# Performance work log

Hardware: AMD Instinct MI355X
Metric: run time of the kernel (lower is better)

## Reference

```python
import jax, jax.numpy as jnp
import numpy as np

N_NODES = 10000
N_EDGES = 256000
H = 128   # n_hidden_feats
P = 64    # n_product_feats
NB = 8    # n_basis
NS = 10   # n_species
RH = 64   # radial MLP hidden width
RC = 5.0  # r_cutoff
AVG = 25.6  # avg_n_neighbors


def _radial(r):
    # Bessel radial basis * polynomial cutoff envelope (p = n_polynomial_cutoff = 5). r: [E,1]
    n = jnp.arange(1, NB + 1, dtype=r.dtype)
    bessel = jnp.sqrt(2.0 / RC) * jnp.sin(n * jnp.pi * r / RC) / r  # [E,NB]
    u = r / RC
    p = 5.0
    env = 1.0 - 0.5 * (p + 1) * (p + 2) * u**p + p * (p + 2) * u**(p + 1) - 0.5 * p * (p + 1) * u**(p + 2)
    env = jnp.where(u < 1.0, env, 0.0)
    return bessel * env


def _mlp(x, Ws):
    for W in Ws[:-1]:
        x = jax.nn.silu(x @ W)
    return x @ Ws[-1]


def _B0(w, A0, A1):
    # correlation-3 symmetric contractions to a scalar target; w: [N,5,P]
    dot = jnp.sum(A1 * A1, axis=-1)  # [N,P]  (rank-1 . rank-1)
    return (w[:, 0] * A0 + w[:, 1] * A0**2 + w[:, 2] * A0**3
            + w[:, 3] * dot + w[:, 4] * A0 * dot)


def _forward(positions, shifts, node_attrs,
             W_embed, Wsc1, Wup0_1, R1_0, R1_1, R1_2, R1_3,
             Wout0_1, Wout1_1, Wp0_1, Wp1_1, Wl0_1, Wl1_1,
             Wsc2, Wup0_2, Wup1_2, R2_0, R2_1, R2_2, R2_3,
             Wout0_2, Wout1_2, Wp0_2, Wl0_2,
             idx_i, idx_j):
    v = positions[idx_i] - positions[idx_j] - shifts                    # [E,3]
    r = jnp.maximum(jnp.linalg.norm(v, axis=-1, keepdims=True), 1e-9)   # [E,1]
    Y1 = v / r                                                          # Cartesian harmonics, l=1
    edge_feats = _radial(r)                                             # [E,NB]

    feats0 = node_attrs @ W_embed                                       # [N,H] scalar node embedding

    # ---- interaction 1: node feats l=0, edge attrs l<=1 -> targets l<=1 ----
    sc0 = jnp.einsum('nk,kch,nc->nh', node_attrs, Wsc1, feats0)         # per-species residual
    h0 = feats0 @ Wup0_1
    w = _mlp(edge_feats, (R1_0, R1_1, R1_2, R1_3)).reshape(-1, 2, H)    # tp weights per edge
    h0j = h0[idx_j]                                                     # [E,H]
    m0 = w[:, 0] * h0j                                                  # 0x0->0
    m1 = (w[:, 1] * h0j)[:, :, None] * Y1[:, None, :]                   # 0x1->1, [E,H,3]
    a0 = jax.ops.segment_sum(m0, idx_i, num_segments=N_NODES) / AVG
    a1 = jax.ops.segment_sum(m1, idx_i, num_segments=N_NODES) / AVG
    A0 = a0 @ Wout0_1                                                   # [N,P]
    A1 = jnp.einsum('nhd,hp->npd', a1, Wout1_1)                         # [N,P,3]

    # ---- product basis 1 (correlation 3, targets l=0 and l=1) ----
    wp0 = jnp.einsum('nk,kqp->nqp', node_attrs, Wp0_1)                  # [N,5,P]
    wp1 = jnp.einsum('nk,kqp->nqp', node_attrs, Wp1_1)                  # [N,4,P]
    B0 = _B0(wp0, A0, A1)
    dot = jnp.sum(A1 * A1, axis=-1)
    B1 = (wp1[:, 0] + wp1[:, 1] * A0 + wp1[:, 2] * A0**2 + wp1[:, 3] * dot)[:, :, None] * A1
    out0 = B0 @ Wl0_1 + sc0                                             # [N,H]
    out1 = jnp.einsum('npd,ph->nhd', B1, Wl1_1)                         # [N,H,3] (sc has no l=1 part)

    # ---- interaction 2: node feats l<=1, targets l<=1; product target l=0 ----
    sc0b = jnp.einsum('nk,kch,nc->nh', node_attrs, Wsc2, out0)
    g0 = out0 @ Wup0_2
    g1 = jnp.einsum('nhd,hg->ngd', out1, Wup1_2)
    w2 = _mlp(edge_feats, (R2_0, R2_1, R2_2, R2_3)).reshape(-1, 5, H)   # 5 tp paths
    g0j = g0[idx_j]
    g1j = g1[idx_j]
    Y1e = Y1[:, None, :]
    m0 = w2[:, 0] * g0j + w2[:, 3] * jnp.sum(g1j * Y1e, axis=-1)        # 0x0->0, 1x1->0 (dot)
    m1 = ((w2[:, 1] * g0j)[:, :, None] * Y1e                             # 0x1->1
          + w2[:, 2][:, :, None] * g1j                                   # 1x0->1
          + w2[:, 4][:, :, None] * jnp.cross(g1j, jnp.broadcast_to(Y1e, g1j.shape)))  # 1x1->1
    a0 = jax.ops.segment_sum(m0, idx_i, num_segments=N_NODES) / AVG
    a1 = jax.ops.segment_sum(m1, idx_i, num_segments=N_NODES) / AVG
    A0 = a0 @ Wout0_2
    A1 = jnp.einsum('nhd,hp->npd', a1, Wout1_2)
    wp0 = jnp.einsum('nk,kqp->nqp', node_attrs, Wp0_2)
    out0b = _B0(wp0, A0, A1) @ Wl0_2 + sc0b                             # [N,H]

    # torch returns [feats[:, :H] per layer]; the first H flattened columns are the scalar block
    return jnp.stack([out0, out0b], axis=0)                             # [2,N,H]


def setup_inputs() -> dict:
    key = jax.random.key(0)
    ks = iter(jax.random.split(key, 40))

    def nrm(shape, fan_in):
        return jax.random.normal(next(ks), shape, dtype=jnp.float32) / np.sqrt(fan_in)

    positions = jax.random.normal(next(ks), (N_NODES, 3), dtype=jnp.float32) * 8.0
    idx_i = jax.random.randint(next(ks), (N_EDGES,), 0, N_NODES)
    idx_j = jax.random.randint(next(ks), (N_EDGES,), 0, N_NODES)
    shifts = jnp.zeros((N_EDGES, 3), jnp.float32)
    species = jax.random.randint(next(ks), (N_NODES,), 0, NS)
    node_attrs = jax.nn.one_hot(species, NS, dtype=jnp.float32)

    return dict(
        positions=positions, shifts=shifts, node_attrs=node_attrs,
        W_embed=nrm((NS, H), NS),
        Wsc1=nrm((NS, H, H), H), Wup0_1=nrm((H, H), H),
        R1_0=nrm((NB, RH), NB), R1_1=nrm((RH, RH), RH), R1_2=nrm((RH, RH), RH), R1_3=nrm((RH, 2 * H), RH),
        Wout0_1=nrm((H, P), H), Wout1_1=nrm((H, P), H),
        Wp0_1=nrm((NS, 5, P), 1.0), Wp1_1=nrm((NS, 4, P), 1.0),
        Wl0_1=nrm((P, H), P), Wl1_1=nrm((P, H), P),
        Wsc2=nrm((NS, H, H), H), Wup0_2=nrm((H, H), H), Wup1_2=nrm((H, H), H),
        R2_0=nrm((NB, RH), NB), R2_1=nrm((RH, RH), RH), R2_2=nrm((RH, RH), RH), R2_3=nrm((RH, 5 * H), RH),
        Wout0_2=nrm((H, P), H), Wout1_2=nrm((H, P), H),
        Wp0_2=nrm((NS, 5, P), 1.0),
        Wl0_2=nrm((P, H), P),
        idx_i=idx_i, idx_j=idx_j,
    )


def reference(positions, shifts, node_attrs,
              W_embed, Wsc1, Wup0_1, R1_0, R1_1, R1_2, R1_3,
              Wout0_1, Wout1_1, Wp0_1, Wp1_1, Wl0_1, Wl1_1,
              Wsc2, Wup0_2, Wup1_2, R2_0, R2_1, R2_2, R2_3,
              Wout0_2, Wout1_2, Wp0_2, Wl0_2,
              idx_i, idx_j):
    return _forward(positions, shifts, node_attrs,
                    W_embed, Wsc1, Wup0_1, R1_0, R1_1, R1_2, R1_3,
                    Wout0_1, Wout1_1, Wp0_1, Wp1_1, Wl0_1, Wl1_1,
                    Wsc2, Wup0_2, Wup1_2, R2_0, R2_1, R2_2, R2_3,
                    Wout0_2, Wout1_2, Wp0_2, Wl0_2,
                    idx_i, idx_j)
```

## Files before the change

kernel.cpp:

```cpp
#include <hip/hip_runtime.h>
#include <math.h>

#define NN 10000
#define NE 256000
#define HD 128
#define PD 64
#define NBASIS 8
#define NSPEC 10
#define RHID 64
#define RCUT 5.0f
#define INV_AVG 0.0390625f
#define PI_F 3.14159265358979f
#define ECAP 12288
#define NACTCAP 8192
#define RSZ 819

__device__ __forceinline__ float silu(float x) {
    return x / (1.0f + expf(-x));
}

__global__ __launch_bounds__(256) void k_initTables(
    const float* __restrict__ na_, const float* __restrict__ We,
    const float* __restrict__ Wsc1, const float* __restrict__ Wup01,
    const float* __restrict__ Wup02, const float* __restrict__ Wsc2,
    int* __restrict__ spec, int* __restrict__ ecnt, int* cnt, int* eTot,
    int* __restrict__ scurG, int* __restrict__ actLst,
    float* __restrict__ sc0s, float* __restrict__ h0s,
    float* __restrict__ g0d, float* __restrict__ sc0bd) {
    __shared__ float ls[HD];
    int b = blockIdx.x;
    if (b < 40) {
        int n = b * 256 + threadIdx.x;
        if (n == 0) { *cnt = 0; *eTot = 0; }
        if (n < NSPEC) scurG[n] = 0;
        if (n < NACTCAP) actLst[n] = -1;
        if (n >= NN) return;
        ecnt[n] = 0;
        int s = 0;
        for (int k = 0; k < NSPEC; k++)
            if (na_[n * NSPEC + k] > 0.5f) s = k;
        spec[n] = s;
    } else {
        int s = b - 40;
        int t = threadIdx.x;
        if (t < HD) {
            float acc1 = 0.f, acc2 = 0.f;
            for (int c = 0; c < HD; c++) {
                float fe = We[s * HD + c];
                acc1 += fe * Wsc1[((size_t)s * HD + c) * HD + t];
                acc2 += fe * Wup01[c * HD + t];
            }
            sc0s[s * HD + t] = acc1;
            h0s[s * HD + t] = acc2;
            ls[t] = acc1;
        }
        __syncthreads();
        if (t < HD) {
            float a1 = 0.f, a2 = 0.f;
            for (int c = 0; c < HD; c++) {
                float v = ls[c];
                a1 += v * Wup02[c * HD + t];
                a2 += v * Wsc2[((size_t)s * HD + c) * HD + t];
            }
            g0d[s * HD + t] = a1;
            sc0bd[s * HD + t] = a2;
        }
    }
}

__global__ __launch_bounds__(256) void k_compact(
    const float* __restrict__ pos, const float* __restrict__ shifts,
    const int* __restrict__ ii, const int* __restrict__ jj,
    int* cnt, int* __restrict__ ecnt,
    int* __restrict__ ui, int* __restrict__ uj,
    float* __restrict__ uY, float* __restrict__ uF) {
    __shared__ int lTot;
    __shared__ int blockBase;
    int t = threadIdx.x;
    if (t == 0) lTot = 0;
    __syncthreads();
    int e0 = (blockIdx.x * 256 + t) * 4;
    int iv[4], jv[4], keep[4];
    float vx[4], vy[4], vz[4], rr[4];
    #pragma unroll
    for (int k = 0; k < 4; k++) {
        int e = e0 + k;
        int i = ii[e], j = jj[e];
        iv[k] = i; jv[k] = j;
        float x = pos[i * 3 + 0] - pos[j * 3 + 0] - shifts[e * 3 + 0];
        float y = pos[i * 3 + 1] - pos[j * 3 + 1] - shifts[e * 3 + 1];
        float z = pos[i * 3 + 2] - pos[j * 3 + 2] - shifts[e * 3 + 2];
        float r = sqrtf(x * x + y * y + z * z);
        r = fmaxf(r, 1e-9f);
        vx[k] = x; vy[k] = y; vz[k] = z; rr[k] = r;
        keep[k] = (r < RCUT) ? 1 : 0;
    }
    int myCnt = keep[0] + keep[1] + keep[2] + keep[3];
    int myOff = 0;
    if (myCnt) myOff = atomicAdd(&lTot, myCnt);
    __syncthreads();
    if (t == 0) blockBase = atomicAdd(cnt, lTot);
    __syncthreads();
    int slot = blockBase + myOff;
    #pragma unroll
    for (int k = 0; k < 4; k++) {
        if (!keep[k]) continue;
        int i = iv[k];
        atomicAdd(&ecnt[i], 1);
        ui[slot] = i; uj[slot] = jv[k];
        float r = rr[k];
        float inv = 1.0f / r;
        uY[slot * 3 + 0] = vx[k] * inv;
        uY[slot * 3 + 1] = vy[k] * inv;
        uY[slot * 3 + 2] = vz[k] * inv;
        float u = r * (1.0f / RCUT);
        float u5 = u * u * u * u * u;
        float env = 1.0f - 21.0f * u5 + 35.0f * u5 * u - 15.0f * u5 * u * u;
        float c0 = 0.6324555320336759f * env * inv;
        float th = PI_F * u;
        float s1, c1;
        __sincosf(th, &s1, &c1);
        float two_c1 = 2.0f * c1;
        float sp = 0.f, sn = s1;
        uF[slot * NBASIS + 0] = c0 * sn;
        #pragma unroll
        for (int b = 1; b < NBASIS; b++) {
            float s_new = two_c1 * sn - sp;
            sp = sn; sn = s_new;
            uF[slot * NBASIS + b] = c0 * sn;
        }
        slot++;
    }
}

__global__ __launch_bounds__(256) void k_assignPlace(
    const int* __restrict__ ecnt, const int* __restrict__ spec,
    int* __restrict__ ebase, int* __restrict__ ecur,
    int* eTot, int* scurG,
    int* __restrict__ actIndex, int* __restrict__ actList) {
    __shared__ int lTot;
    __shared__ int blockBase;
    __shared__ int lHist[NSPEC];
    __shared__ int lBase[NSPEC];
    int t = threadIdx.x;
    int n = blockIdx.x * 256 + t;
    if (t == 0) lTot = 0;
    if (t < NSPEC) lHist[t] = 0;
    __syncthreads();
    int ec = (n < NN) ? ecnt[n] : 0;
    int s = (n < NN) ? spec[n] : 0;
    bool act = (ec > 0);
    int myOff = 0, myIdx = 0;
    if (act) {
        myOff = atomicAdd(&lTot, ec);
        myIdx = atomicAdd(&lHist[s], 1);
    }
    __syncthreads();
    if (t == 0) blockBase = atomicAdd(eTot, lTot);
    if (t < NSPEC) lBase[t] = (lHist[t] > 0) ? atomicAdd(&scurG[t], lHist[t]) : 0;
    __syncthreads();
    if (n < NN) {
        if (act) {
            int b = blockBase + myOff;
            ebase[n] = b;
            ecur[n] = b;
            int rank = lBase[s] + myIdx;
            if (rank < RSZ) {
                int p = s * RSZ + rank;
                actList[p] = n;
                actIndex[n] = p;
            } else {
                actIndex[n] = -1;
            }
        } else {
            actIndex[n] = -1;
        }
    }
}

__global__ __launch_bounds__(256) void k_sortFill(
    const int* cnt, const int* __restrict__ ui, const int* __restrict__ uj,
    const float* __restrict__ uY, const float* __restrict__ uF,
    int* __restrict__ ecur, int* __restrict__ sj,
    float* __restrict__ sY, float* __restrict__ sF,
    const int* __restrict__ spec, const float* __restrict__ sc0s,
    const float* __restrict__ sc0bd,
    float* __restrict__ out0g, float* __restrict__ outbg) {
    int b = blockIdx.x;
    if (b < 48) {
        int e = b * 256 + threadIdx.x;
        int n = *cnt; if (n > ECAP) n = ECAP;
        if (e >= n) return;
        int slot = atomicAdd(&ecur[ui[e]], 1);
        if (slot >= ECAP) return;
        sj[slot] = uj[e];
        #pragma unroll
        for (int d = 0; d < 3; d++) sY[slot * 3 + d] = uY[e * 3 + d];
        #pragma unroll
        for (int bb = 0; bb < NBASIS; bb++) sF[slot * NBASIS + bb] = uF[e * NBASIS + bb];
    } else {
        int t = (b - 48) * 256 + threadIdx.x;
        int n = t >> 6, c = t & 63;
        if (n >= NN) return;
        int s = spec[n];
        out0g[(size_t)n * HD + c] = sc0s[s * HD + c];
        out0g[(size_t)n * HD + 64 + c] = sc0s[s * HD + 64 + c];
        outbg[(size_t)n * HD + c] = sc0bd[s * HD + c];
        outbg[(size_t)n * HD + 64 + c] = sc0bd[s * HD + 64 + c];
    }
}

__global__ __launch_bounds__(256) void k_hid(
    const int* cnt, const float* __restrict__ sF,
    const float* __restrict__ A0, const float* __restrict__ A1, const float* __restrict__ A2,
    const float* __restrict__ B0, const float* __restrict__ B1, const float* __restrict__ B2,
    float* __restrict__ xh1, float* __restrict__ xh2) {
    int lane = threadIdx.x & 63;
    int wid = (blockIdx.x * 256 + threadIdx.x) >> 6;
    int ne = *cnt; if (ne > ECAP) ne = ECAP;
    int base = wid * 2;
    if (base >= ne) return;
    const float* W0 = (blockIdx.y == 0) ? A0 : B0;
    const float* W1 = (blockIdx.y == 0) ? A1 : B1;
    const float* W2 = (blockIdx.y == 0) ? A2 : B2;
    float* dst = (blockIdx.y == 0) ? xh1 : xh2;
    int e0 = base, e1 = (base + 1 < ne) ? base + 1 : base;
    float x0, x1;
    {
        float F0[NBASIS], F1[NBASIS];
        #pragma unroll
        for (int b = 0; b < NBASIS; b++) { F0[b] = sF[e0 * NBASIS + b]; F1[b] = sF[e1 * NBASIS + b]; }
        float a0 = 0.f, a1 = 0.f;
        #pragma unroll
        for (int b = 0; b < NBASIS; b++) {
            float wv = W0[b * RHID + lane];
            a0 += F0[b] * wv; a1 += F1[b] * wv;
        }
        x0 = silu(a0); x1 = silu(a1);
    }
    {
        float c0 = 0.f, c1 = 0.f;
        for (int c = 0; c < RHID; c++) {
            float wv = W1[c * RHID + lane];
            c0 += __shfl(x0, c) * wv; c1 += __shfl(x1, c) * wv;
        }
        x0 = silu(c0); x1 = silu(c1);
    }
    {
        float c0 = 0.f, c1 = 0.f;
        for (int c = 0; c < RHID; c++) {
            float wv = W2[c * RHID + lane];
            c0 += __shfl(x0, c) * wv; c1 += __shfl(x1, c) * wv;
        }
        x0 = silu(c0); x1 = silu(c1);
    }
    dst[(size_t)e0 * RHID + lane] = x0;
    if (base + 1 < ne) dst[(size_t)e1 * RHID + lane] = x1;
}

__global__ __launch_bounds__(256) void k_wmat(
    const int* cnt, const float* __restrict__ xh1, const float* __restrict__ xh2,
    const float* __restrict__ A3, const float* __restrict__ B3,
    float* __restrict__ ew1, float* __restrict__ ew2) {
    __shared__ float sX[32 * RHID];
    int lane = threadIdx.x & 63;
    int w = __builtin_amdgcn_readfirstlane((int)(threadIdx.x >> 6));
    int y = blockIdx.y;
    int ne = *cnt; if (ne > ECAP) ne = ECAP;
    const float* X; const float* W; float* dst; int ncol, col0;
    if (y < 4) { X = xh1; W = A3; dst = ew1; ncol = 2 * HD; col0 = y * 64; }
    else       { X = xh2; W = B3; dst = ew2; ncol = 5 * HD; col0 = (y - 4) * 64; }
    int eBase = blockIdx.x * 32;
    {
        const float4* src = (const float4*)(X + (size_t)eBase * RHID);
        float4* d4 = (float4*)sX;
        #pragma unroll
        for (int it = 0; it < 2; it++)
            d4[threadIdx.x + it * 256] = src[threadIdx.x + it * 256];
    }
    __syncthreads();
    if (eBase >= ne) return;
    int w8 = w * 8;
    float acc[8] = {0,0,0,0,0,0,0,0};
    for (int c = 0; c < RHID; c += 4) {
        float4 xv[8];
        #pragma unroll
        for (int k = 0; k < 8; k++) xv[k] = *(const float4*)&sX[(w8 + k) * RHID + c];
        #pragma unroll
        for (int cc = 0; cc < 4; cc++) {
            float wv = W[(c + cc) * ncol + col0 + lane];
            #pragma unroll
            for (int k = 0; k < 8; k++) {
                float xc = (cc==0)?xv[k].x:(cc==1)?xv[k].y:(cc==2)?xv[k].z:xv[k].w;
                acc[k] += xc * wv;
            }
        }
    }
    int e0 = eBase + w8;
    int rem = ne - e0; if (rem > 8) rem = 8;
    for (int k = 0; k < rem; k++)
        dst[(size_t)(e0 + k) * ncol + col0 + lane] = acc[k];
}

__global__ __launch_bounds__(256) void k_agg1(
    const int* __restrict__ actList,
    const int* __restrict__ ebase, const int* __restrict__ ecnt,
    const int* __restrict__ sj, const float* __restrict__ sY,
    const float* __restrict__ ew, const int* __restrict__ spec,
    const float* __restrict__ h0s, float* __restrict__ a0c, float* __restrict__ a1c) {
    int lane = threadIdx.x & 63;
    int ia = (blockIdx.x * 256 + threadIdx.x) >> 6;
    int h = blockIdx.y * 64;
    int n = actList[ia];
    if (n < 0) return;
    int eb = ebase[n], ec = ecnt[n];
    float a0 = 0.f;
    float a1[3] = {0,0,0};
    for (int idx = eb; idx < eb + ec; idx++) {
        int j = sj[idx];
        int sp = spec[j];
        float h0 = h0s[sp * HD + h + lane];
        const float* w = ew + (size_t)idx * 256;
        float w0 = w[h + lane], w1 = w[128 + h + lane];
        a0 += w0 * h0;
        float m1 = w1 * h0;
        #pragma unroll
        for (int d = 0; d < 3; d++) a1[d] += m1 * sY[idx * 3 + d];
    }
    a0c[(size_t)ia * HD + h + lane] = a0 * INV_AVG;
    #pragma unroll
    for (int d = 0; d < 3; d++)
        a1c[((size_t)d * NACTCAP + ia) * HD + h + lane] = a1[d] * INV_AVG;
}

__global__ __launch_bounds__(256) void k_proj(
    const int* __restrict__ actList,
    const float* __restrict__ x0buf, const float* __restrict__ x1buf,
    const float* __restrict__ W0, const float* __restrict__ W1,
    float* __restrict__ am0, float* __restrict__ am1) {
    __shared__ float sX[16 * HD];
    int lane = threadIdx.x & 63;
    int w = __builtin_amdgcn_readfirstlane((int)(threadIdx.x >> 6));
    int y = blockIdx.y;
    const float* X = (y == 0) ? x0buf : (x1buf + (size_t)(y - 1) * NACTCAP * HD);
    const float* W = (y == 0) ? W0 : W1;
    int iaBase = blockIdx.x * 16;
    {
        const float4* src = (const float4*)(X + (size_t)iaBase * HD);
        float4* d4 = (float4*)sX;
        #pragma unroll
        for (int it = 0; it < 2; it++)
            d4[threadIdx.x + it * 256] = src[threadIdx.x + it * 256];
    }
    __syncthreads();
    bool any = false;
    int ia0 = iaBase + w * 4;
    #pragma unroll
    for (int k = 0; k < 4; k++) any = any || (actList[ia0 + k] >= 0);
    if (!any) return;
    float* dst = (y == 0) ? am0 : (am1 + (size_t)(y - 1) * NACTCAP * PD);
    int w4 = w * 4;
    float acc[4] = {0,0,0,0};
    for (int c = 0; c < HD; c += 4) {
        float4 xv[4];
        #pragma unroll
        for (int k = 0; k < 4; k++) xv[k] = *(const float4*)&sX[(w4 + k) * HD + c];
        #pragma unroll
        for (int cc = 0; cc < 4; cc++) {
            float wv = W[(c + cc) * PD + lane];
            #pragma unroll
            for (int k = 0; k < 4; k++) {
                float xc = (cc==0)?xv[k].x:(cc==1)?xv[k].y:(cc==2)?xv[k].z:xv[k].w;
                acc[k] += xc * wv;
            }
        }
    }
    #pragma unroll
    for (int k = 0; k < 4; k++) dst[(size_t)(ia0 + k) * PD + lane] = acc[k];
}

__global__ __launch_bounds__(256) void k_bout(
    const int* __restrict__ actList,
    const float* __restrict__ am0, const float* __restrict__ am1,
    const int* __restrict__ spec,
    const float* __restrict__ Wp0, const float* __restrict__ Wp1,
    const float* __restrict__ Wl0, const float* __restrict__ Wl1,
    const float* __restrict__ sc0s,
    float* __restrict__ out0g, float* __restrict__ out0c, float* __restrict__ out1c) {
    __shared__ float sB[4][8][PD];
    int lane = threadIdx.x & 63;
    int w = __builtin_amdgcn_readfirstlane((int)(threadIdx.x >> 6));
    int y = blockIdx.y;
    int bs = y >> 1, h = (y & 1) * 64;
    int ia0 = (blockIdx.x * 4 + w) * 8;
    int nv[8], sk[8];
    bool any = false;
    #pragma unroll
    for (int k = 0; k < 8; k++) {
        nv[k] = actList[ia0 + k];
        any = any || (nv[k] >= 0);
        sk[k] = spec[(nv[k] >= 0) ? nv[k] : 0];
    }
    if (!any) return;
    #pragma unroll
    for (int k = 0; k < 8; k++) {
        int ia = ia0 + k;
        int s = sk[k];
        float A0v = am0[(size_t)ia * PD + lane];
        float a1x = am1[((size_t)0 * NACTCAP + ia) * PD + lane];
        float a1y = am1[((size_t)1 * NACTCAP + ia) * PD + lane];
        float a1z = am1[((size_t)2 * NACTCAP + ia) * PD + lane];
        float dot = a1x * a1x + a1y * a1y + a1z * a1z;
        float A02 = A0v * A0v;
        float B;
        if (bs == 0) {
            const float* wp = Wp0 + (size_t)(s * 5) * PD;
            B = wp[lane] * A0v + wp[PD + lane] * A02 + wp[2 * PD + lane] * A02 * A0v +
                wp[3 * PD + lane] * dot + wp[4 * PD + lane] * A0v * dot;
        } else {
            const float* wp = Wp1 + (size_t)(s * 4) * PD;
            float fac = wp[lane] + wp[PD + lane] * A0v + wp[2 * PD + lane] * A02 + wp[3 * PD + lane] * dot;
            float a1d = (bs == 1) ? a1x : ((bs == 2) ? a1y : a1z);
            B = fac * a1d;
        }
        sB[w][k][lane] = B;
    }
    const float* Wl = (bs == 0) ? Wl0 : Wl1;
    float o[8] = {0,0,0,0,0,0,0,0};
    for (int q = 0; q < PD; q += 4) {
        float4 bq[8];
        #pragma unroll
        for (int k = 0; k < 8; k++) bq[k] = *(const float4*)&sB[w][k][q];
        #pragma unroll
        for (int qq = 0; qq < 4; qq++) {
            float wl = Wl[(q + qq) * HD + h + lane];
            #pragma unroll
            for (int k = 0; k < 8; k++) {
                float b = (qq==0)?bq[k].x:(qq==1)?bq[k].y:(qq==2)?bq[k].z:bq[k].w;
                o[k] += b * wl;
            }
        }
    }
    if (bs == 0) {
        #pragma unroll
        for (int k = 0; k < 8; k++) {
            int ia = ia0 + k;
            float v = o[k] + sc0s[sk[k] * HD + h + lane];
            if (nv[k] >= 0) out0g[(size_t)nv[k] * HD + h + lane] = v;
            out0c[(size_t)ia * HD + h + lane] = v;
        }
    } else {
        float* dst = out1c + (size_t)(bs - 1) * NACTCAP * HD;
        #pragma unroll
        for (int k = 0; k < 8; k++)
            dst[(size_t)(ia0 + k) * HD + h + lane] = o[k];
    }
}

__global__ __launch_bounds__(256) void k_g(
    const int* __restrict__ actList, const int* __restrict__ spec,
    const float* __restrict__ out0c, const float* __restrict__ out1c,
    const float* __restrict__ Wsc2, const float* __restrict__ Wup02, const float* __restrict__ Wup12,
    float* __restrict__ sc0bc, float* __restrict__ g0c, float* __restrict__ g1c) {
    __shared__ float sX[32 * HD];
    int lane = threadIdx.x & 63;
    int w = __builtin_amdgcn_readfirstlane((int)(threadIdx.x >> 6));
    int y = blockIdx.y;
    int st = y >> 1, h = (y & 1) * 64;
    int blockBase = blockIdx.x * 32;
    const float* X = (st <= 1) ? out0c : (out1c + (size_t)(st - 2) * NACTCAP * HD);
    {
        const float4* src = (const float4*)(X + (size_t)blockBase * HD);
        float4* d4 = (float4*)sX;
        #pragma unroll
        for (int it = 0; it < 4; it++)
            d4[threadIdx.x + it * 256] = src[threadIdx.x + it * 256];
    }
    int nb0 = actList[blockBase];
    int sB0 = spec[(nb0 >= 0) ? nb0 : 0];
    __syncthreads();
    int ia0 = blockBase + w * 8;
    int nv[8], sk[8];
    bool any = false;
    #pragma unroll
    for (int k = 0; k < 8; k++) {
        nv[k] = actList[ia0 + k];
        any = any || (nv[k] >= 0);
        sk[k] = (st == 0) ? spec[(nv[k] >= 0) ? nv[k] : 0] : 0;
    }
    if (!any) return;
    const float* Wt = (st == 0) ? (Wsc2 + (size_t)sB0 * HD * HD)
                    : ((st == 1) ? Wup02 : Wup12);
    int w8 = w * 8;
    float acc[8] = {0,0,0,0,0,0,0,0};
    for (int c = 0; c < HD; c += 4) {
        float4 xv[8];
        #pragma unroll
        for (int k = 0; k < 8; k++) xv[k] = *(const float4*)&sX[(w8 + k) * HD + c];
        #pragma unroll
        for (int cc = 0; cc < 4; cc++) {
            float wv = Wt[(c + cc) * HD + h + lane];
            #pragma unroll
            for (int k = 0; k < 8; k++) {
                float xc = (cc==0)?xv[k].x:(cc==1)?xv[k].y:(cc==2)?xv[k].z:xv[k].w;
                acc[k] += xc * wv;
            }
        }
    }
    if (st == 0) {
        #pragma unroll 1
        for (int k = 0; k < 8; k++) {
            if (nv[k] < 0 || sk[k] == sB0) continue;
            const float* Wm = Wsc2 + (size_t)sk[k] * HD * HD;
            float p = 0.f;
            for (int c = 0; c < HD; c++) p += sX[(w8 + k) * HD + c] * Wm[c * HD + h + lane];
            acc[k] = p;
        }
    }
    float* dst = (st == 0) ? sc0bc : ((st == 1) ? g0c : (g1c + (size_t)(st - 2) * NACTCAP * HD));
    #pragma unroll
    for (int k = 0; k < 8; k++)
        dst[(size_t)(ia0 + k) * HD + h + lane] = acc[k];
}

__global__ __launch_bounds__(256) void k_agg2(
    const int* __restrict__ actList,
    const int* __restrict__ ebase, const int* __restrict__ ecnt,
    const int* __restrict__ sj, const float* __restrict__ sY,
    const float* __restrict__ ew, const int* __restrict__ spec,
    const int* __restrict__ actIndex,
    const float* __restrict__ g0c, const float* __restrict__ g1c,
    const float* __restrict__ g0d,
    float* __restrict__ a0c, float* __restrict__ a1c) {
    int lane = threadIdx.x & 63;
    int ia = (blockIdx.x * 256 + threadIdx.x) >> 6;
    int h = blockIdx.y * 64;
    int n = actList[ia];
    if (n < 0) return;
    int eb = ebase[n], ec = ecnt[n];
    float m0 = 0.f;
    float s1[3] = {0,0,0};
    for (int idx = eb; idx < eb + ec; idx++) {
        int j = sj[idx];
        float Yx = sY[idx * 3 + 0], Yy = sY[idx * 3 + 1], Yz = sY[idx * 3 + 2];
        int ji = actIndex[j];
        float gv, gx, gy, gz;
        if (ji >= 0) {
            gv = g0c[(size_t)ji * HD + h + lane];
            gx = g1c[((size_t)0 * NACTCAP + ji) * HD + h + lane];
            gy = g1c[((size_t)1 * NACTCAP + ji) * HD + h + lane];
            gz = g1c[((size_t)2 * NACTCAP + ji) * HD + h + lane];
        } else {
            gv = g0d[spec[j] * HD + h + lane];
            gx = gy = gz = 0.f;
        }
        const float* wr = ew + (size_t)idx * 640;
        float w0 = wr[h + lane];
        float w1 = wr[128 + h + lane];
        float w2 = wr[256 + h + lane];
        float w3 = wr[384 + h + lane];
        float w4 = wr[512 + h + lane];
        float dot = gx * Yx + gy * Yy + gz * Yz;
        m0 += w0 * gv + w3 * dot;
        float cx = gy * Yz - gz * Yy, cy = gz * Yx - gx * Yz, cz = gx * Yy - gy * Yx;
        s1[0] += w1 * gv * Yx + w2 * gx + w4 * cx;
        s1[1] += w1 * gv * Yy + w2 * gy + w4 * cy;
        s1[2] += w1 * gv * Yz + w2 * gz + w4 * cz;
    }
    a0c[(size_t)ia * HD + h + lane] = m0 * INV_AVG;
    #pragma unroll
    for (int d = 0; d < 3; d++)
        a1c[((size_t)d * NACTCAP + ia) * HD + h + lane] = s1[d] * INV_AVG;
}

__global__ __launch_bounds__(256) void k_outC(
    const int* __restrict__ actList, const int* __restrict__ spec,
    const float* __restrict__ am0, const float* __restrict__ am1,
    const float* __restrict__ Wp0, const float* __restrict__ Wl0,
    const float* __restrict__ sc0bc, float* __restrict__ outbg) {
    __shared__ float sB[4][8][PD];
    int lane = threadIdx.x & 63;
    int w = __builtin_amdgcn_readfirstlane((int)(threadIdx.x >> 6));
    int h = blockIdx.y * 64;
    int ia0 = (blockIdx.x * 4 + w) * 8;
    int nv[8];
    bool any = false;
    #pragma unroll
    for (int k = 0; k < 8; k++) { nv[k] = actList[ia0 + k]; any = any || (nv[k] >= 0); }
    if (!any) return;
    #pragma unroll
    for (int k = 0; k < 8; k++) {
        int ia = ia0 + k;
        int s = spec[(nv[k] >= 0) ? nv[k] : 0];
        float A0v = am0[(size_t)ia * PD + lane];
        float a1x = am1[((size_t)0 * NACTCAP + ia) * PD + lane];
        float a1y = am1[((size_t)1 * NACTCAP + ia) * PD + lane];
        float a1z = am1[((size_t)2 * NACTCAP + ia) * PD + lane];
        float dot = a1x * a1x + a1y * a1y + a1z * a1z;
        float A02 = A0v * A0v;
        const float* wp = Wp0 + (size_t)(s * 5) * PD;
        sB[w][k][lane] = wp[lane] * A0v + wp[PD + lane] * A02 + wp[2 * PD + lane] * A02 * A0v +
                         wp[3 * PD + lane] * dot + wp[4 * PD + lane] * A0v * dot;
    }
    float o[8] = {0,0,0,0,0,0,0,0};
    for (int q = 0; q < PD; q += 4) {
        float4 bq[8];
        #pragma unroll
        for (int k = 0; k < 8; k++) bq[k] = *(const float4*)&sB[w][k][q];
        #pragma unroll
        for (int qq = 0; qq < 4; qq++) {
            float wl = Wl0[(q + qq) * HD + h + lane];
            #pragma unroll
            for (int k = 0; k < 8; k++) {
                float b = (qq==0)?bq[k].x:(qq==1)?bq[k].y:(qq==2)?bq[k].z:bq[k].w;
                o[k] += b * wl;
            }
        }
    }
    #pragma unroll
    for (int k = 0; k < 8; k++) {
        if (nv[k] < 0) continue;
        int ia = ia0 + k;
        outbg[(size_t)nv[k] * HD + h + lane] = o[k] + sc0bc[(size_t)ia * HD + h + lane];
    }
}

extern "C" void kernel_launch(void* const* d_in, const int* in_sizes, int n_in,
                              void* d_out, int out_size, void* d_ws, size_t ws_size,
                              hipStream_t stream) {
    const float* pos    = (const float*)d_in[0];
    const float* shifts = (const float*)d_in[1];
    const float* na     = (const float*)d_in[2];
    const float* We     = (const float*)d_in[3];
    const float* Wsc1   = (const float*)d_in[4];
    const float* Wup01  = (const float*)d_in[5];
    const float* R10    = (const float*)d_in[6];
    const float* R11    = (const float*)d_in[7];
    const float* R12    = (const float*)d_in[8];
    const float* R13    = (const float*)d_in[9];
    const float* Wout01 = (const float*)d_in[10];
    const float* Wout11 = (const float*)d_in[11];
    const float* Wp01   = (const float*)d_in[12];
    const float* Wp11   = (const float*)d_in[13];
    const float* Wl01   = (const float*)d_in[14];
    const float* Wl11   = (const float*)d_in[15];
    const float* Wsc2   = (const float*)d_in[16];
    const float* Wup02  = (const float*)d_in[17];
    const float* Wup12  = (const float*)d_in[18];
    const float* R20    = (const float*)d_in[19];
    const float* R21    = (const float*)d_in[20];
    const float* R22    = (const float*)d_in[21];
    const float* R23    = (const float*)d_in[22];
    const float* Wout02 = (const float*)d_in[23];
    const float* Wout12 = (const float*)d_in[24];
    const float* Wp02   = (const float*)d_in[25];
    const float* Wl02   = (const float*)d_in[26];
    const int*   idx_i  = (const int*)d_in[27];
    const int*   idx_j  = (const int*)d_in[28];
    float* out = (float*)d_out;
    float* outb = out + (size_t)NN * HD;

    char* ws = (char*)d_ws;
    size_t off = 0;
    auto alloc = [&](size_t bytes) -> char* {
        char* pp = ws + off;
        off += (bytes + 255) & ~(size_t)255;
        return pp;
    };
    int*   cnt    = (int*)alloc(4);
    int*   eTot   = (int*)alloc(4);
    int*   scurG  = (int*)alloc(NSPEC * 4);
    int*   spec   = (int*)alloc((size_t)NN * 4);
    int*   ecnt   = (int*)alloc((size_t)NN * 4);
    int*   ebase  = (int*)alloc((size_t)NN * 4);
    int*   ecur   = (int*)alloc((size_t)NN * 4);
    int*   actIdx = (int*)alloc((size_t)NN * 4);
    int*   actLst = (int*)alloc((size_t)NACTCAP * 4);
    float* sc0s   = (float*)alloc((size_t)NSPEC * HD * 4);
    float* h0s    = (float*)alloc((size_t)NSPEC * HD * 4);
    float* g0d    = (float*)alloc((size_t)NSPEC * HD * 4);
    float* sc0bd  = (float*)alloc((size_t)NSPEC * HD * 4);
    int*   sj     = (int*)alloc((size_t)ECAP * 4);
    float* sYv    = (float*)alloc((size_t)ECAP * 3 * 4);
    float* sFv    = (float*)alloc((size_t)ECAP * NBASIS * 4);
    float* xh1    = (float*)alloc((size_t)ECAP * RHID * 4);
    float* xh2    = (float*)alloc((size_t)ECAP * RHID * 4);
    float* ew1    = (float*)alloc((size_t)ECAP * 256 * 4);
    float* ew2    = (float*)alloc((size_t)ECAP * 640 * 4);
    int*   ui     = (int*)ew2;
    int*   uj     = ui + NE;
    float* uY     = (float*)(uj + NE);
    float* uF     = uY + (size_t)NE * 3;
    float* a0c    = (float*)alloc((size_t)NACTCAP * HD * 4);
    float* a1c    = (float*)alloc((size_t)NACTCAP * HD * 3 * 4);
    float* am0    = (float*)alloc((size_t)NACTCAP * PD * 4);
    float* am1    = (float*)alloc((size_t)NACTCAP * PD * 3 * 4);
    float* out0c  = (float*)alloc((size_t)NACTCAP * HD * 4);
    float* out1c  = (float*)alloc((size_t)NACTCAP * HD * 3 * 4);
    float* g0c    = (float*)alloc((size_t)NACTCAP * HD * 4);
    float* g1c    = (float*)alloc((size_t)NACTCAP * HD * 3 * 4);
    float* sc0bc  = (float*)alloc((size_t)NACTCAP * HD * 4);

    k_initTables<<<50, 256, 0, stream>>>(na, We, Wsc1, Wup01, Wup02, Wsc2,
                                         spec, ecnt, cnt, eTot, scurG, actLst,
                                         sc0s, h0s, g0d, sc0bd);
    k_compact<<<NE / 1024, 256, 0, stream>>>(pos, shifts, idx_i, idx_j, cnt, ecnt,
                                             ui, uj, uY, uF);
    k_assignPlace<<<(NN + 255) / 256, 256, 0, stream>>>(ecnt, spec, ebase, ecur,
                                                        eTot, scurG, actIdx, actLst);
    k_sortFill<<<48 + (NN * 64) / 256, 256, 0, stream>>>(cnt, ui, uj, uY, uF, ecur,
                                                         sj, sYv, sFv,
                                                         spec, sc0s, sc0bd, out, outb);
    k_hid<<<dim3(ECAP / 8, 2), 256, 0, stream>>>(cnt, sFv, R10, R11, R12,
                                                 R20, R21, R22, xh1, xh2);
    k_wmat<<<dim3(ECAP / 32, 14), 256, 0, stream>>>(cnt, xh1, xh2, R13, R23, ew1, ew2);
    k_agg1<<<dim3(NACTCAP / 4, 2), 256, 0, stream>>>(actLst, ebase, ecnt, sj, sYv, ew1,
                                                     spec, h0s, a0c, a1c);
    k_proj<<<dim3(NACTCAP / 16, 4), 256, 0, stream>>>(actLst, a0c, a1c, Wout01, Wout11,
                                                      am0, am1);
    k_bout<<<dim3(NACTCAP / 32, 8), 256, 0, stream>>>(actLst, am0, am1, spec,
                                                      Wp01, Wp11, Wl01, Wl11, sc0s,
                                                      out, out0c, out1c);
    k_g<<<dim3(NACTCAP / 32, 10), 256, 0, stream>>>(actLst, spec, out0c, out1c,
                                                    Wsc2, Wup02, Wup12, sc0bc, g0c, g1c);
    k_agg2<<<dim3(NACTCAP / 4, 2), 256, 0, stream>>>(actLst, ebase, ecnt, sj, sYv, ew2,
                                                     spec, actIdx, g0c, g1c, g0d, a0c, a1c);
    k_proj<<<dim3(NACTCAP / 16, 4), 256, 0, stream>>>(actLst, a0c, a1c, Wout02, Wout12,
                                                      am0, am1);
    k_outC<<<dim3(NACTCAP / 32, 2), 256, 0, stream>>>(actLst, spec, am0, am1, Wp02, Wl02,
                                                      sc0bc, outb);
}
```

Baseline: 190.7 us.

## Register-tile the wmat and g GEMMs with 4x8 per-thread blocks

Both small dense-GEMM kernels (radial-weight output layer and the second-layer node linear maps) switch from one column per lane with 8 rows per wave to a 4-row by 8-column register tile per thread. Each block now covers 64 rows and 128 columns, X is staged into padded shared memory, and weights are read as float4. This is meant to raise arithmetic intensity and cut redundant weight loads and launch count. In k_g the mixed-species fallback now runs block-wide only when the block is not species-homogeneous, which adds serial per-row work in that case.

```diff
diff --git a/kernel.cpp b/kernel.cpp
--- a/kernel.cpp
+++ b/kernel.cpp
@@ -262,44 +262,51 @@
     const int* cnt, const float* __restrict__ xh1, const float* __restrict__ xh2,
     const float* __restrict__ A3, const float* __restrict__ B3,
     float* __restrict__ ew1, float* __restrict__ ew2) {
-    __shared__ float sX[32 * RHID];
-    int lane = threadIdx.x & 63;
-    int w = __builtin_amdgcn_readfirstlane((int)(threadIdx.x >> 6));
+    __shared__ float sX[64 * 65];
+    int t = threadIdx.x;
+    int ne = *cnt; if (ne > ECAP) ne = ECAP;
     int y = blockIdx.y;
-    int ne = *cnt; if (ne > ECAP) ne = ECAP;
+    int eBase = blockIdx.x * 64;
+    if (eBase >= ne) return;
     const float* X; const float* W; float* dst; int ncol, col0;
-    if (y < 4) { X = xh1; W = A3; dst = ew1; ncol = 2 * HD; col0 = y * 64; }
-    else       { X = xh2; W = B3; dst = ew2; ncol = 5 * HD; col0 = (y - 4) * 64; }
-    int eBase = blockIdx.x * 32;
+    if (y < 2) { X = xh1; W = A3; dst = ew1; ncol = 2 * HD; col0 = y * 128; }
+    else       { X = xh2; W = B3; dst = ew2; ncol = 5 * HD; col0 = (y - 2) * 128; }
     {
         const float4* src = (const float4*)(X + (size_t)eBase * RHID);
-        float4* d4 = (float4*)sX;
-        #pragma unroll
-        for (int it = 0; it < 2; it++)
-            d4[threadIdx.x + it * 256] = src[threadIdx.x + it * 256];
-    }
-    __syncthreads();
-    if (eBase >= ne) return;
-    int w8 = w * 8;
-    float acc[8] = {0,0,0,0,0,0,0,0};
-    for (int c = 0; c < RHID; c += 4) {
-        float4 xv[8];
-        #pragma unroll
-        for (int k = 0; k < 8; k++) xv[k] = *(const float4*)&sX[(w8 + k) * RHID + c];
-        #pragma unroll
-        for (int cc = 0; cc < 4; cc++) {
-            float wv = W[(c + cc) * ncol + col0 + lane];
+        #pragma unroll
+        for (int it = 0; it < 4; it++) {
+            int idx = t + it * 256;
+            float4 v = src[idx];
+            int e = idx >> 4, c4 = (idx & 15) * 4;
+            float* d = &sX[e * 65 + c4];
+            d[0] = v.x; d[1] = v.y; d[2] = v.z; d[3] = v.w;
+        }
+    }
+    __syncthreads();
+    int sgrp = t >> 4;
+    int cg = col0 + (t & 15) * 8;
+    float acc[4][8] = {};
+    for (int c = 0; c < RHID; c++) {
+        float xk[4];
+        #pragma unroll
+        for (int k = 0; k < 4; k++) xk[k] = sX[(sgrp * 4 + k) * 65 + c];
+        float4 wA = *(const float4*)(W + (size_t)c * ncol + cg);
+        float4 wB = *(const float4*)(W + (size_t)c * ncol + cg + 4);
+        float wv[8] = {wA.x, wA.y, wA.z, wA.w, wB.x, wB.y, wB.z, wB.w};
+        #pragma unroll
+        for (int k = 0; k < 4; k++)
             #pragma unroll
-            for (int k = 0; k < 8; k++) {
-                float xc = (cc==0)?xv[k].x:(cc==1)?xv[k].y:(cc==2)?xv[k].z:xv[k].w;
-                acc[k] += xc * wv;
-            }
-        }
-    }
-    int e0 = eBase + w8;
-    int rem = ne - e0; if (rem > 8) rem = 8;
-    for (int k = 0; k < rem; k++)
-        dst[(size_t)(e0 + k) * ncol + col0 + lane] = acc[k];
+            for (int q = 0; q < 8; q++)
+                acc[k][q] += xk[k] * wv[q];
+    }
+    #pragma unroll
+    for (int k = 0; k < 4; k++) {
+        int e = eBase + sgrp * 4 + k;
+        *(float4*)(dst + (size_t)e * ncol + cg) =
+            make_float4(acc[k][0], acc[k][1], acc[k][2], acc[k][3]);
+        *(float4*)(dst + (size_t)e * ncol + cg + 4) =
+            make_float4(acc[k][4], acc[k][5], acc[k][6], acc[k][7]);
+    }
 }
 
 __global__ __launch_bounds__(256) void k_agg1(
@@ -462,65 +469,83 @@
     const float* __restrict__ out0c, const float* __restrict__ out1c,
     const float* __restrict__ Wsc2, const float* __restrict__ Wup02, const float* __restrict__ Wup12,
     float* __restrict__ sc0bc, float* __restrict__ g0c, float* __restrict__ g1c) {
-    __shared__ float sX[32 * HD];
-    int lane = threadIdx.x & 63;
-    int w = __builtin_amdgcn_readfirstlane((int)(threadIdx.x >> 6));
-    int y = blockIdx.y;
-    int st = y >> 1, h = (y & 1) * 64;
-    int blockBase = blockIdx.x * 32;
+    __shared__ float sX[64 * 129];
+    __shared__ int sSpec[64];
+    __shared__ int sB0, sAny, sMis;
+    int t = threadIdx.x;
+    int st = blockIdx.y;
+    int slotBase = blockIdx.x * 64;
     const float* X = (st <= 1) ? out0c : (out1c + (size_t)(st - 2) * NACTCAP * HD);
+    if (t < 64) {
+        int n = actList[slotBase + t];
+        sSpec[t] = (n >= 0) ? spec[n] : -1;
+    }
+    __syncthreads();
+    if (t == 0) {
+        int sb = 0, any = 0, mis = 0;
+        for (int k = 0; k < 64; k++) {
+            int sv = sSpec[k];
+            if (sv >= 0) {
+                if (!any) { sb = sv; any = 1; }
+                else if (sv != sb) mis = 1;
+            }
+        }
+        sB0 = sb; sAny = any; sMis = mis;
+    }
+    __syncthreads();
+    if (!sAny) return;
     {
-        const float4* src = (const float4*)(X + (size_t)blockBase * HD);
-        float4* d4 = (float4*)sX;
-        #pragma unroll
-        for (int it = 0; it < 4; it++)
-            d4[threadIdx.x + it * 256] = src[threadIdx.x + it * 256];
-    }
-    int nb0 = actList[blockBase];
-    int sB0 = spec[(nb0 >= 0) ? nb0 : 0];
-    __syncthreads();
-    int ia0 = blockBase + w * 8;
-    int nv[8], sk[8];
-    bool any = false;
-    #pragma unroll
-    for (int k = 0; k < 8; k++) {
-        nv[k] = actList[ia0 + k];
-        any = any || (nv[k] >= 0);
-        sk[k] = (st == 0) ? spec[(nv[k] >= 0) ? nv[k] : 0] : 0;
-    }
-    if (!any) return;
+        const float4* src = (const float4*)(X + (size_t)slotBase * HD);
+        #pragma unroll
+        for (int it = 0; it < 8; it++) {
+            int idx = t + it * 256;
+            float4 v = src[idx];
+            int e = idx >> 5, c4 = (idx & 31) * 4;
+            float* d = &sX[e * 129 + c4];
+            d[0] = v.x; d[1] = v.y; d[2] = v.z; d[3] = v.w;
+        }
+    }
+    __syncthreads();
     const float* Wt = (st == 0) ? (Wsc2 + (size_t)sB0 * HD * HD)
                     : ((st == 1) ? Wup02 : Wup12);
-    int w8 = w * 8;
-    float acc[8] = {0,0,0,0,0,0,0,0};
-    for (int c = 0; c < HD; c += 4) {
-        float4 xv[8];
-        #pragma unroll
-        for (int k = 0; k < 8; k++) xv[k] = *(const float4*)&sX[(w8 + k) * HD + c];
-        #pragma unroll
-        for (int cc = 0; cc < 4; cc++) {
-            float wv = Wt[(c + cc) * HD + h + lane];
+    float* dst = (st == 0) ? sc0bc : ((st == 1) ? g0c : (g1c + (size_t)(st - 2) * NACTCAP * HD));
+    int sgrp = t >> 4;
+    int cg = (t & 15) * 8;
+    float acc[4][8] = {};
+    for (int c = 0; c < HD; c++) {
+        float xk[4];
+        #pragma unroll
+        for (int k = 0; k < 4; k++) xk[k] = sX[(sgrp * 4 + k) * 129 + c];
+        float4 wA = *(const float4*)(Wt + (size_t)c * HD + cg);
+        float4 wB = *(const float4*)(Wt + (size_t)c * HD + cg + 4);
+        float wv[8] = {wA.x, wA.y, wA.z, wA.w, wB.x, wB.y, wB.z, wB.w};
+        #pragma unroll
+        for (int k = 0; k < 4; k++)
             #pragma unroll
-            for (int k = 0; k < 8; k++) {
-                float xc = (cc==0)?xv[k].x:(cc==1)?xv[k].y:(cc==2)?xv[k].z:xv[k].w;
-                acc[k] += xc * wv;
+            for (int q = 0; q < 8; q++)
+                acc[k][q] += xk[k] * wv[q];
+    }
+    #pragma unroll
+    for (int k = 0; k < 4; k++) {
+        int slot = slotBase + sgrp * 4 + k;
+        *(float4*)(dst + (size_t)slot * HD + cg) =
+            make_float4(acc[k][0], acc[k][1], acc[k][2], acc[k][3]);
+        *(float4*)(dst + (size_t)slot * HD + cg + 4) =
+            make_float4(acc[k][4], acc[k][5], acc[k][6], acc[k][7]);
+    }
+    if (st == 0 && sMis) {
+        __syncthreads();
+        for (int k = 0; k < 64; k++) {
+            int sv = sSpec[k];
+            if (sv < 0 || sv == sB0) continue;
+            if (t < HD) {
+                const float* Wm = Wsc2 + (size_t)sv * HD * HD;
+                float p = 0.f;
+                for (int c = 0; c < HD; c++) p += sX[k * 129 + c] * Wm[c * HD + t];
+                sc0bc[(size_t)(slotBase + k) * HD + t] = p;
             }
         }
     }
-    if (st == 0) {
-        #pragma unroll 1
-        for (int k = 0; k < 8; k++) {
-            if (nv[k] < 0 || sk[k] == sB0) continue;
-            const float* Wm = Wsc2 + (size_t)sk[k] * HD * HD;
-            float p = 0.f;
-            for (int c = 0; c < HD; c++) p += sX[(w8 + k) * HD + c] * Wm[c * HD + h + lane];
-            acc[k] = p;
-        }
-    }
-    float* dst = (st == 0) ? sc0bc : ((st == 1) ? g0c : (g1c + (size_t)(st - 2) * NACTCAP * HD));
-    #pragma unroll
-    for (int k = 0; k < 8; k++)
-        dst[(size_t)(ia0 + k) * HD + h + lane] = acc[k];
 }
 
 __global__ __launch_bounds__(256) void k_agg2(
@@ -713,7 +738,7 @@
                                                          spec, sc0s, sc0bd, out, outb);
     k_hid<<<dim3(ECAP / 8, 2), 256, 0, stream>>>(cnt, sFv, R10, R11, R12,
                                                  R20, R21, R22, xh1, xh2);
-    k_wmat<<<dim3(ECAP / 32, 14), 256, 0, stream>>>(cnt, xh1, xh2, R13, R23, ew1, ew2);
+    k_wmat<<<dim3(ECAP / 64, 7), 256, 0, stream>>>(cnt, xh1, xh2, R13, R23, ew1, ew2);
     k_agg1<<<dim3(NACTCAP / 4, 2), 256, 0, stream>>>(actLst, ebase, ecnt, sj, sYv, ew1,
                                                      spec, h0s, a0c, a1c);
     k_proj<<<dim3(NACTCAP / 16, 4), 256, 0, stream>>>(actLst, a0c, a1c, Wout01, Wout11,
@@ -721,8 +746,8 @@
     k_bout<<<dim3(NACTCAP / 32, 8), 256, 0, stream>>>(actLst, am0, am1, spec,
                                                       Wp01, Wp11, Wl01, Wl11, sc0s,
                                                       out, out0c, out1c);
-    k_g<<<dim3(NACTCAP / 32, 10), 256, 0, stream>>>(actLst, spec, out0c, out1c,
-                                                    Wsc2, Wup02, Wup12, sc0bc, g0c, g1c);
+    k_g<<<dim3(NACTCAP / 64, 5), 256, 0, stream>>>(actLst, spec, out0c, out1c,
+                                                   Wsc2, Wup02, Wup12, sc0bc, g0c, g1c);
     k_agg2<<<dim3(NACTCAP / 4, 2), 256, 0, stream>>>(actLst, ebase, ecnt, sj, sYv, ew2,
                                                      spec, actIdx, g0c, g1c, g0d, a0c, a1c);
     k_proj<<<dim3(NACTCAP / 16, 4), 256, 0, stream>>>(actLst, a0c, a1c, Wout02, Wout12,
```

Result: faster. 176.8 us (-7.3%).
